# Optimization experiments

Hardware: AMD Instinct MI355X
Metric: run time of the kernel (lower is better)

The kernel has to match this reference:

```python
import jax, jax.numpy as jnp
import numpy as np

B, L, F, T = 512, 512, 128, 512

def setup_inputs() -> dict:
    key = jax.random.key(0)
    ks = jax.random.split(key, 8)
    s_ih = 1.0 / np.sqrt(L)
    return {
        "h0": jax.random.normal(ks[0], (1, B, L), jnp.float32),
        "c0": jax.random.normal(ks[1], (1, B, L), jnp.float32),
        "W_ih": jax.random.normal(ks[2], (4 * L, F), jnp.float32) * s_ih,
        "W_hh": jax.random.normal(ks[3], (4 * L, L), jnp.float32) * s_ih,
        "b_ih": jax.random.normal(ks[4], (4 * L,), jnp.float32) * s_ih,
        "b_hh": jax.random.normal(ks[5], (4 * L,), jnp.float32) * s_ih,
        "W_dense": jax.random.normal(ks[6], (F, L), jnp.float32) * s_ih,
        "b_dense": jax.random.normal(ks[7], (F,), jnp.float32) * s_ih,
        "seq_len": T,
    }

def reference(h0, c0, W_ih, W_hh, b_ih, b_hh, W_dense, b_dense, seq_len):
    h = h0[0]  # [B, L] (squeeze num_layers dim)
    c = c0[0]
    x = h @ W_dense.T + b_dense  # initial x_i = dense(h)

    def step(carry, _):
        x, h, c = carry
        gates = x @ W_ih.T + b_ih + h @ W_hh.T + b_hh  # [B, 4L]
        i, f, g, o = jnp.split(gates, 4, axis=-1)
        c2 = jax.nn.sigmoid(f) * c + jax.nn.sigmoid(i) * jnp.tanh(g)
        h2 = jax.nn.sigmoid(o) * jnp.tanh(c2)
        x2 = h2 @ W_dense.T + b_dense  # [B, F]
        return (x2, h2, c2), x2

    _, xs = jax.lax.scan(step, (x, h, c), None, length=seq_len)  # xs: [T, B, F]
    # torch code cats along axis=1 then views (-1, seq_len, n_features) -> [B, T, F]
    return jnp.transpose(xs, (1, 0, 2))
```

## Files before the change

kernel.cpp:

```cpp
#include <hip/hip_runtime.h>
#include <hip/hip_fp16.h>

#define T_STEPS 512
#define BDIM 512
#define LDIM 512
#define FDIM 128

typedef _Float16 half8 __attribute__((ext_vector_type(8)));
typedef float f4_t __attribute__((ext_vector_type(4)));

#define OFF_WPERM   0u
#define OFF_WDH     2097152u
#define OFF_BCOMB   2228224u
#define OFF_HBUF0   2236416u
#define OFF_HBUF1   2760704u
#define OFF_FLAGS   3284992u

__device__ __forceinline__ float sigmoidf_(float x) { return 1.f / (1.f + __expf(-x)); }
__device__ __forceinline__ float tanhf_(float x) { return 1.f - 2.f / (__expf(2.f * x) + 1.f); }

__device__ __forceinline__ void gload_lds16(const void* g, void* l) {
    __builtin_amdgcn_global_load_lds(
        (const __attribute__((address_space(1))) void*)g,
        (__attribute__((address_space(3))) void*)l, 16, 0, 0);
}

__device__ __forceinline__ unsigned long long aload64(const void* p) {
    return __hip_atomic_load((unsigned long long*)p, __ATOMIC_RELAXED, __HIP_MEMORY_SCOPE_AGENT);
}
__device__ __forceinline__ unsigned aload32(const void* p) {
    return __hip_atomic_load((unsigned*)p, __ATOMIC_RELAXED, __HIP_MEMORY_SCOPE_AGENT);
}
__device__ __forceinline__ void astore32(void* p, unsigned v) {
    __hip_atomic_store((unsigned*)p, v, __ATOMIC_RELAXED, __HIP_MEMORY_SCOPE_AGENT);
}

__global__ __launch_bounds__(256) void k_prep_w(
    const float* __restrict__ W_ih, const float* __restrict__ W_hh,
    const float* __restrict__ b_ih, const float* __restrict__ b_hh,
    const float* __restrict__ W_dense, const float* __restrict__ b_dense,
    _Float16* __restrict__ Wperm, float* __restrict__ bcomb)
{
    __shared__ float ih[FDIM];
    const int pr = blockIdx.x;
    const int gate = pr & 3, sg = pr >> 2;
    const int j = gate * 512 + sg;
    const int tid = threadIdx.x;
    if (tid < FDIM) ih[tid] = W_ih[j * FDIM + tid];
    __syncthreads();
    const int k0 = tid * 2;
    float a0 = W_hh[(size_t)j * LDIM + k0];
    float a1 = W_hh[(size_t)j * LDIM + k0 + 1];
    for (int f = 0; f < FDIM; ++f) {
        const float w = ih[f];
        a0 += w * W_dense[f * LDIM + k0];
        a1 += w * W_dense[f * LDIM + k0 + 1];
    }
    const int s = (pr & 7) << 6;
    Wperm[(size_t)pr * LDIM + (k0 ^ s)] = (_Float16)a0;
    Wperm[(size_t)pr * LDIM + (k0 ^ s) + 1] = (_Float16)a1;
    if (tid == 0) {
        float acc = b_ih[j] + b_hh[j];
        for (int f = 0; f < FDIM; ++f) acc += ih[f] * b_dense[f];
        bcomb[j] = acc;
    }
}

__global__ __launch_bounds__(256) void k_prep_misc(
    const float* __restrict__ W_dense, const float* __restrict__ h0,
    _Float16* __restrict__ Wdh, _Float16* __restrict__ hbuf0)
{
    const int bid = blockIdx.x, tid = threadIdx.x;
    const int k0 = tid * 2;
    if (bid < FDIM) {
        const int f = bid; const int s = (f & 7) << 6;
        Wdh[f * LDIM + (k0 ^ s)] = (_Float16)W_dense[f * LDIM + k0];
        Wdh[f * LDIM + (k0 ^ s) + 1] = (_Float16)W_dense[f * LDIM + k0 + 1];
    } else {
        const int r = bid - FDIM; const int s = (r & 7) << 6;
        hbuf0[r * LDIM + (k0 ^ s)] = (_Float16)h0[r * LDIM + k0];
        hbuf0[r * LDIM + (k0 ^ s) + 1] = (_Float16)h0[r * LDIM + k0 + 1];
    }
}

#define LDS_W   0
#define LDS_WD  65536
#define LDS_H   69632
#define LDS_TOT 135168

__device__ __forceinline__ void stage_h(char* smem, const char* gh, int tid) {
    #pragma unroll
    for (int ch = 0; ch < 4; ++ch) {
        unsigned long long tmp[8];
        #pragma unroll
        for (int r = 0; r < 8; ++r) tmp[r] = aload64(gh + ((ch * 8 + r) * 256 + tid) * 8);
        #pragma unroll
        for (int r = 0; r < 8; ++r)
            *(unsigned long long*)(smem + LDS_H + ((ch * 8 + r) * 256 + tid) * 8) = tmp[r];
    }
}

__global__ __launch_bounds__(256, 1) void k_persist(
    const _Float16* __restrict__ Wperm, const _Float16* __restrict__ Wdh,
    const float* __restrict__ bcomb, const float* __restrict__ bdense,
    const float* __restrict__ c0,
    _Float16* __restrict__ hb0, _Float16* __restrict__ hb1,
    float* __restrict__ out, unsigned* __restrict__ flags)
{
    __shared__ __align__(16) char smem[LDS_TOT];
    const int cb = blockIdx.x;
    const int g = blockIdx.y;
    const int tid = threadIdx.x;
    const int w = tid >> 6, lane = tid & 63;
    const int wm = w >> 1, wn = w & 1;
    const int lr = lane & 15, lh = lane >> 4;

    {
        const char* gw = (const char*)Wperm + (size_t)cb * 65536;
        #pragma unroll
        for (int i = 0; i < 16; ++i)
            gload_lds16(gw + (i * 256 + tid) * 16, smem + LDS_W + (i * 256 + tid) * 16);
        const char* gd = (const char*)Wdh + (size_t)cb * 4096;
        gload_lds16(gd + tid * 16, smem + LDS_WD + tid * 16);
    }

    float bi[2], bf[2], bg[2], bo[2];
    float creg[2][2];
    #pragma unroll
    for (int mt2 = 0; mt2 < 2; ++mt2) {
        const int sg = cb * 16 + 8 * wm + 4 * mt2 + lh;
        bi[mt2] = bcomb[0 * 512 + sg];
        bf[mt2] = bcomb[1 * 512 + sg];
        bg[mt2] = bcomb[2 * 512 + sg];
        bo[mt2] = bcomb[3 * 512 + sg];
        #pragma unroll
        for (int nt2 = 0; nt2 < 2; ++nt2) {
            const int row = g * 64 + (2 * wn + nt2) * 16 + lr;
            creg[mt2][nt2] = c0[(size_t)row * LDIM + sg];
        }
    }
    float bd[4];
    #pragma unroll
    for (int j = 0; j < 4; ++j) bd[j] = bdense[cb * 4 + j];

    const int ntx = 2 * wn + wm;
    const int swz = (lr & 7) << 7;
    const int swD = ((cb * 4 + lr) & 7) << 7;
    const char* pA0 = smem + LDS_W + ((2 * wm + 0) * 16 + lr) * 1024;
    const char* pA1 = smem + LDS_W + ((2 * wm + 1) * 16 + lr) * 1024;
    const char* pB0 = smem + LDS_H + ((2 * wn + 0) * 16 + lr) * 1024;
    const char* pB1 = smem + LDS_H + ((2 * wn + 1) * 16 + lr) * 1024;
    const char* pBx = smem + LDS_H + (ntx * 16 + lr) * 1024;
    const char* pD  = smem + LDS_WD + lr * 1024;

    unsigned* myflags = flags + g * 32;

    stage_h(smem, (const char*)hb0 + (size_t)g * 65536, tid);
    __syncthreads();

    half8 aA0[16], aA1[16], aD[16];
    #pragma unroll
    for (int kt = 0; kt < 16; ++kt) {
        const int kb = kt * 64 + lh * 16;
        aA0[kt] = *(const half8*)(pA0 + (kb ^ swz));
        aA1[kt] = *(const half8*)(pA1 + (kb ^ swz));
        aD[kt]  = *(const half8*)(pD  + (kb ^ swD));
    }

    for (int t = 1; t <= T_STEPS; ++t) {
        char* hout = (char*)((t & 1) ? hb1 : hb0);

        f4_t acc[2][2] = {};
        f4_t accx = {};
        #pragma unroll
        for (int kt = 0; kt < 16; ++kt) {
            const int kb = kt * 64 + lh * 16;
            const half8 b0 = *(const half8*)(pB0 + (kb ^ swz));
            const half8 b1 = *(const half8*)(pB1 + (kb ^ swz));
            acc[0][0] = __builtin_amdgcn_mfma_f32_16x16x32_f16(aA0[kt], b0, acc[0][0], 0, 0, 0);
            acc[0][1] = __builtin_amdgcn_mfma_f32_16x16x32_f16(aA0[kt], b1, acc[0][1], 0, 0, 0);
            acc[1][0] = __builtin_amdgcn_mfma_f32_16x16x32_f16(aA1[kt], b0, acc[1][0], 0, 0, 0);
            acc[1][1] = __builtin_amdgcn_mfma_f32_16x16x32_f16(aA1[kt], b1, acc[1][1], 0, 0, 0);
            accx = __builtin_amdgcn_mfma_f32_16x16x32_f16(aD[kt], wm ? b1 : b0, accx, 0, 0, 0);
        }

        #pragma unroll
        for (int mt2 = 0; mt2 < 2; ++mt2) {
            const int sg = cb * 16 + 8 * wm + 4 * mt2 + lh;
            #pragma unroll
            for (int nt2 = 0; nt2 < 2; ++nt2) {
                const int row = g * 64 + (2 * wn + nt2) * 16 + lr;
                const float iv = sigmoidf_(acc[mt2][nt2][0] + bi[mt2]);
                const float fv = sigmoidf_(acc[mt2][nt2][1] + bf[mt2]);
                const float gv = tanhf_(acc[mt2][nt2][2] + bg[mt2]);
                const float ov = sigmoidf_(acc[mt2][nt2][3] + bo[mt2]);
                const float cnew = fv * creg[mt2][nt2] + iv * gv;
                const float hnew = ov * tanhf_(cnew);
                creg[mt2][nt2] = cnew;
                const unsigned u = (unsigned)__builtin_bit_cast(unsigned short, (_Float16)hnew);
                const unsigned up = (unsigned)__shfl_xor((int)u, 16);
                if ((lh & 1) == 0) {
                    const unsigned word = u | (up << 16);
                    astore32(hout + row * 1024 + ((sg * 2) ^ ((row & 7) << 7)), word);
                }
            }
        }

        __syncthreads();
        if (tid == 0) astore32(myflags + cb, (unsigned)t);

        if (t >= 2 && lh == 0) {
            const int row = g * 64 + ntx * 16 + lr;
            float* o = &out[((size_t)row * T_STEPS + (t - 2)) * FDIM + cb * 4];
            o[0] = accx[0] + bd[0];
            o[1] = accx[1] + bd[1];
            o[2] = accx[2] + bd[2];
            o[3] = accx[3] + bd[3];
        }

        if (w == 0) {
            for (;;) {
                const unsigned v = (lane < 32) ? aload32(myflags + lane) : 0xffffffffu;
                if (__all(v >= (unsigned)t)) break;
                __builtin_amdgcn_s_sleep(1);
            }
        }
        __syncthreads();

        stage_h(smem, (const char*)((t & 1) ? hb1 : hb0) + (size_t)g * 65536, tid);
        __syncthreads();
    }

    {
        f4_t accx = {};
        #pragma unroll
        for (int kt = 0; kt < 16; ++kt) {
            const int kb = kt * 64 + lh * 16;
            const half8 b = *(const half8*)(pBx + (kb ^ swz));
            accx = __builtin_amdgcn_mfma_f32_16x16x32_f16(aD[kt], b, accx, 0, 0, 0);
        }
        if (lh == 0) {
            const int row = g * 64 + ntx * 16 + lr;
            float* o = &out[((size_t)row * T_STEPS + (T_STEPS - 1)) * FDIM + cb * 4];
            o[0] = accx[0] + bd[0];
            o[1] = accx[1] + bd[1];
            o[2] = accx[2] + bd[2];
            o[3] = accx[3] + bd[3];
        }
    }
}

extern "C" void kernel_launch(void* const* d_in, const int* in_sizes, int n_in,
                              void* d_out, int out_size, void* d_ws, size_t ws_size,
                              hipStream_t stream)
{
    const float* h0      = (const float*)d_in[0];
    const float* c0      = (const float*)d_in[1];
    const float* W_ih    = (const float*)d_in[2];
    const float* W_hh    = (const float*)d_in[3];
    const float* b_ih    = (const float*)d_in[4];
    const float* b_hh    = (const float*)d_in[5];
    const float* W_dense = (const float*)d_in[6];
    const float* b_dense = (const float*)d_in[7];
    float* out = (float*)d_out;
    char* ws = (char*)d_ws;

    _Float16* Wperm = (_Float16*)(ws + OFF_WPERM);
    _Float16* Wdh   = (_Float16*)(ws + OFF_WDH);
    float*    bcomb = (float*)(ws + OFF_BCOMB);
    _Float16* hb0   = (_Float16*)(ws + OFF_HBUF0);
    _Float16* hb1   = (_Float16*)(ws + OFF_HBUF1);
    unsigned* flags = (unsigned*)(ws + OFF_FLAGS);

    hipMemsetAsync(flags, 0, 1024, stream);
    k_prep_w<<<2048, 256, 0, stream>>>(W_ih, W_hh, b_ih, b_hh, W_dense, b_dense, Wperm, bcomb);
    k_prep_misc<<<FDIM + BDIM, 256, 0, stream>>>(W_dense, h0, Wdh, hb0);
    k_persist<<<dim3(32, 8), 256, 0, stream>>>(Wperm, Wdh, bcomb, b_dense, c0, hb0, hb1, out, flags);
}
```

Before: 2.838 ms.

## Replace block-wide barrier sync with per-wave flags and direct register h loads

Drops LDS staging of the hidden state and the two block-wide barriers per step. Each wave now owns 16 batch rows across all 64 gate columns and keeps the weights in registers. It waits on per-wave flags published by the 32 column blocks, then loads its h row directly from global memory in four chunks, pipelining the flag check and load of the next chunk behind the MFMAs on the current one. Chunk order is staggered by block to spread contention. The aim is finer-grained sync and less LDS traffic, at the cost of more register pressure and more global polling traffic.

After: 4.982 ms. +75.5%, slower.

```diff
diff --git a/kernel.cpp b/kernel.cpp
--- a/kernel.cpp
+++ b/kernel.cpp
@@ -8,6 +8,7 @@
 
 typedef _Float16 half8 __attribute__((ext_vector_type(8)));
 typedef float f4_t __attribute__((ext_vector_type(4)));
+typedef unsigned long long ull2 __attribute__((ext_vector_type(2)));
 
 #define OFF_WPERM   0u
 #define OFF_WDH     2097152u
@@ -19,17 +20,8 @@
 __device__ __forceinline__ float sigmoidf_(float x) { return 1.f / (1.f + __expf(-x)); }
 __device__ __forceinline__ float tanhf_(float x) { return 1.f - 2.f / (__expf(2.f * x) + 1.f); }
 
-__device__ __forceinline__ void gload_lds16(const void* g, void* l) {
-    __builtin_amdgcn_global_load_lds(
-        (const __attribute__((address_space(1))) void*)g,
-        (__attribute__((address_space(3))) void*)l, 16, 0, 0);
-}
-
 __device__ __forceinline__ unsigned long long aload64(const void* p) {
-    return __hip_atomic_load((unsigned long long*)p, __ATOMIC_RELAXED, __HIP_MEMORY_SCOPE_AGENT);
-}
-__device__ __forceinline__ unsigned aload32(const void* p) {
-    return __hip_atomic_load((unsigned*)p, __ATOMIC_RELAXED, __HIP_MEMORY_SCOPE_AGENT);
+    return __hip_atomic_load((const unsigned long long*)p, __ATOMIC_RELAXED, __HIP_MEMORY_SCOPE_AGENT);
 }
 __device__ __forceinline__ void astore32(void* p, unsigned v) {
     __hip_atomic_store((unsigned*)p, v, __ATOMIC_RELAXED, __HIP_MEMORY_SCOPE_AGENT);
@@ -83,23 +75,6 @@
     }
 }
 
-#define LDS_W   0
-#define LDS_WD  65536
-#define LDS_H   69632
-#define LDS_TOT 135168
-
-__device__ __forceinline__ void stage_h(char* smem, const char* gh, int tid) {
-    #pragma unroll
-    for (int ch = 0; ch < 4; ++ch) {
-        unsigned long long tmp[8];
-        #pragma unroll
-        for (int r = 0; r < 8; ++r) tmp[r] = aload64(gh + ((ch * 8 + r) * 256 + tid) * 8);
-        #pragma unroll
-        for (int r = 0; r < 8; ++r)
-            *(unsigned long long*)(smem + LDS_H + ((ch * 8 + r) * 256 + tid) * 8) = tmp[r];
-    }
-}
-
 __global__ __launch_bounds__(256, 1) void k_persist(
     const _Float16* __restrict__ Wperm, const _Float16* __restrict__ Wdh,
     const float* __restrict__ bcomb, const float* __restrict__ bdense,
@@ -107,140 +82,158 @@
     _Float16* __restrict__ hb0, _Float16* __restrict__ hb1,
     float* __restrict__ out, unsigned* __restrict__ flags)
 {
-    __shared__ __align__(16) char smem[LDS_TOT];
     const int cb = blockIdx.x;
     const int g = blockIdx.y;
     const int tid = threadIdx.x;
-    const int w = tid >> 6, lane = tid & 63;
-    const int wm = w >> 1, wn = w & 1;
+    const int wv = tid >> 6, lane = tid & 63;
     const int lr = lane & 15, lh = lane >> 4;
-
+    const int row = g * 64 + wv * 16 + lr;
+    const int swz = (lr & 7) << 7;
+    const int qs = cb >> 3;
+
+    half8 aA[4][16];
+    half8 aD[16];
     {
-        const char* gw = (const char*)Wperm + (size_t)cb * 65536;
-        #pragma unroll
-        for (int i = 0; i < 16; ++i)
-            gload_lds16(gw + (i * 256 + tid) * 16, smem + LDS_W + (i * 256 + tid) * 16);
-        const char* gd = (const char*)Wdh + (size_t)cb * 4096;
-        gload_lds16(gd + tid * 16, smem + LDS_WD + tid * 16);
-    }
-
-    float bi[2], bf[2], bg[2], bo[2];
-    float creg[2][2];
+        const char* wbase = (const char*)Wperm + (size_t)cb * 65536;
+        const int fd = cb * 4 + (lr & 3);
+        const char* dbase = (const char*)Wdh + (size_t)fd * 1024;
+        const int swD = (fd & 7) << 7;
+        #pragma unroll
+        for (int j = 0; j < 4; ++j) {
+            #pragma unroll
+            for (int cc = 0; cc < 4; ++cc) {
+                const int kt = ((qs + j) & 3) * 4 + cc;
+                const int kb = kt * 64 + lh * 16;
+                const int i = j * 4 + cc;
+                #pragma unroll
+                for (int m = 0; m < 4; ++m)
+                    aA[m][i] = *(const half8*)(wbase + (m * 16 + lr) * 1024 + (kb ^ swz));
+                aD[i] = *(const half8*)(dbase + (kb ^ swD));
+            }
+        }
+    }
+
+    float bi[4], bf[4], bg[4], bo[4], creg[4];
     #pragma unroll
-    for (int mt2 = 0; mt2 < 2; ++mt2) {
-        const int sg = cb * 16 + 8 * wm + 4 * mt2 + lh;
-        bi[mt2] = bcomb[0 * 512 + sg];
-        bf[mt2] = bcomb[1 * 512 + sg];
-        bg[mt2] = bcomb[2 * 512 + sg];
-        bo[mt2] = bcomb[3 * 512 + sg];
-        #pragma unroll
-        for (int nt2 = 0; nt2 < 2; ++nt2) {
-            const int row = g * 64 + (2 * wn + nt2) * 16 + lr;
-            creg[mt2][nt2] = c0[(size_t)row * LDIM + sg];
-        }
+    for (int m = 0; m < 4; ++m) {
+        const int sg = cb * 16 + m * 4 + lh;
+        bi[m] = bcomb[0 * 512 + sg];
+        bf[m] = bcomb[1 * 512 + sg];
+        bg[m] = bcomb[2 * 512 + sg];
+        bo[m] = bcomb[3 * 512 + sg];
+        creg[m] = c0[(size_t)row * LDIM + sg];
     }
     float bd[4];
     #pragma unroll
     for (int j = 0; j < 4; ++j) bd[j] = bdense[cb * 4 + j];
 
-    const int ntx = 2 * wn + wm;
-    const int swz = (lr & 7) << 7;
-    const int swD = ((cb * 4 + lr) & 7) << 7;
-    const char* pA0 = smem + LDS_W + ((2 * wm + 0) * 16 + lr) * 1024;
-    const char* pA1 = smem + LDS_W + ((2 * wm + 1) * 16 + lr) * 1024;
-    const char* pB0 = smem + LDS_H + ((2 * wn + 0) * 16 + lr) * 1024;
-    const char* pB1 = smem + LDS_H + ((2 * wn + 1) * 16 + lr) * 1024;
-    const char* pBx = smem + LDS_H + (ntx * 16 + lr) * 1024;
-    const char* pD  = smem + LDS_WD + lr * 1024;
-
-    unsigned* myflags = flags + g * 32;
-
-    stage_h(smem, (const char*)hb0 + (size_t)g * 65536, tid);
-    __syncthreads();
-
-    half8 aA0[16], aA1[16], aD[16];
-    #pragma unroll
-    for (int kt = 0; kt < 16; ++kt) {
-        const int kb = kt * 64 + lh * 16;
-        aA0[kt] = *(const half8*)(pA0 + (kb ^ swz));
-        aA1[kt] = *(const half8*)(pA1 + (kb ^ swz));
-        aD[kt]  = *(const half8*)(pD  + (kb ^ swD));
-    }
+    unsigned* fbase = flags + (g * 4 + wv) * 32;
+    const size_t rowoff = (size_t)row * 1024;
+
+    unsigned long long pf0, pf1, pf2, pf3;
+    ull2 bq[4], bn[4];
+
+#define FISSUE(q) do { const int qq_ = (q) & 3;                      \
+        pf0 = aload64(fbase + qq_ * 8 + 0);                          \
+        pf1 = aload64(fbase + qq_ * 8 + 2);                          \
+        pf2 = aload64(fbase + qq_ * 8 + 4);                          \
+        pf3 = aload64(fbase + qq_ * 8 + 6); } while (0)
+
+#define FCHECK(q, tw_) do { const int qq_ = (q) & 3;                 \
+        for (;;) {                                                   \
+            if ((unsigned)pf0 >= (tw_) && (unsigned)(pf0 >> 32) >= (tw_) && \
+                (unsigned)pf1 >= (tw_) && (unsigned)(pf1 >> 32) >= (tw_) && \
+                (unsigned)pf2 >= (tw_) && (unsigned)(pf2 >> 32) >= (tw_) && \
+                (unsigned)pf3 >= (tw_) && (unsigned)(pf3 >> 32) >= (tw_)) break; \
+            __builtin_amdgcn_s_sleep(1);                             \
+            pf0 = aload64(fbase + qq_ * 8 + 0);                      \
+            pf1 = aload64(fbase + qq_ * 8 + 2);                      \
+            pf2 = aload64(fbase + qq_ * 8 + 4);                      \
+            pf3 = aload64(fbase + qq_ * 8 + 6);                      \
+        } } while (0)
+
+#define BISSUE(q, dst) do { const int qq_ = (q) & 3;                 \
+        const unsigned dep_ = (unsigned)(((pf0 | pf1 | pf2 | pf3) >> 63) & 1ull); \
+        _Pragma("unroll")                                            \
+        for (int cc_ = 0; cc_ < 4; ++cc_) {                          \
+            const char* hp_ = hbase + rowoff + ((((qq_ * 4 + cc_) * 64 + lh * 16) ^ swz) + dep_); \
+            dst[cc_].x = aload64(hp_);                               \
+            dst[cc_].y = aload64(hp_ + 8); } } while (0)
 
     for (int t = 1; t <= T_STEPS; ++t) {
+        const char* hbase = (const char*)(((t - 1) & 1) ? hb1 : hb0);
         char* hout = (char*)((t & 1) ? hb1 : hb0);
-
-        f4_t acc[2][2] = {};
+        const unsigned tw = (unsigned)(t - 1);
+
+        f4_t acc[4] = {};
         f4_t accx = {};
-        #pragma unroll
-        for (int kt = 0; kt < 16; ++kt) {
-            const int kb = kt * 64 + lh * 16;
-            const half8 b0 = *(const half8*)(pB0 + (kb ^ swz));
-            const half8 b1 = *(const half8*)(pB1 + (kb ^ swz));
-            acc[0][0] = __builtin_amdgcn_mfma_f32_16x16x32_f16(aA0[kt], b0, acc[0][0], 0, 0, 0);
-            acc[0][1] = __builtin_amdgcn_mfma_f32_16x16x32_f16(aA0[kt], b1, acc[0][1], 0, 0, 0);
-            acc[1][0] = __builtin_amdgcn_mfma_f32_16x16x32_f16(aA1[kt], b0, acc[1][0], 0, 0, 0);
-            acc[1][1] = __builtin_amdgcn_mfma_f32_16x16x32_f16(aA1[kt], b1, acc[1][1], 0, 0, 0);
-            accx = __builtin_amdgcn_mfma_f32_16x16x32_f16(aD[kt], wm ? b1 : b0, accx, 0, 0, 0);
-        }
-
-        #pragma unroll
-        for (int mt2 = 0; mt2 < 2; ++mt2) {
-            const int sg = cb * 16 + 8 * wm + 4 * mt2 + lh;
+
+        FISSUE(qs); FCHECK(qs, tw); BISSUE(qs, bq);
+        FISSUE(qs + 1);
+
+        #pragma unroll
+        for (int j = 0; j < 4; ++j) {
+            if (j < 3) {
+                FCHECK(qs + j + 1, tw);
+                BISSUE(qs + j + 1, bn);
+                if (j < 2) FISSUE(qs + j + 2);
+            }
             #pragma unroll
-            for (int nt2 = 0; nt2 < 2; ++nt2) {
-                const int row = g * 64 + (2 * wn + nt2) * 16 + lr;
-                const float iv = sigmoidf_(acc[mt2][nt2][0] + bi[mt2]);
-                const float fv = sigmoidf_(acc[mt2][nt2][1] + bf[mt2]);
-                const float gv = tanhf_(acc[mt2][nt2][2] + bg[mt2]);
-                const float ov = sigmoidf_(acc[mt2][nt2][3] + bo[mt2]);
-                const float cnew = fv * creg[mt2][nt2] + iv * gv;
-                const float hnew = ov * tanhf_(cnew);
-                creg[mt2][nt2] = cnew;
-                const unsigned u = (unsigned)__builtin_bit_cast(unsigned short, (_Float16)hnew);
-                const unsigned up = (unsigned)__shfl_xor((int)u, 16);
-                if ((lh & 1) == 0) {
-                    const unsigned word = u | (up << 16);
-                    astore32(hout + row * 1024 + ((sg * 2) ^ ((row & 7) << 7)), word);
-                }
-            }
-        }
-
-        __syncthreads();
-        if (tid == 0) astore32(myflags + cb, (unsigned)t);
+            for (int cc = 0; cc < 4; ++cc) {
+                const half8 b = __builtin_bit_cast(half8, bq[cc]);
+                const int i = j * 4 + cc;
+                acc[0] = __builtin_amdgcn_mfma_f32_16x16x32_f16(aA[0][i], b, acc[0], 0, 0, 0);
+                acc[1] = __builtin_amdgcn_mfma_f32_16x16x32_f16(aA[1][i], b, acc[1], 0, 0, 0);
+                acc[2] = __builtin_amdgcn_mfma_f32_16x16x32_f16(aA[2][i], b, acc[2], 0, 0, 0);
+                acc[3] = __builtin_amdgcn_mfma_f32_16x16x32_f16(aA[3][i], b, acc[3], 0, 0, 0);
+                accx   = __builtin_amdgcn_mfma_f32_16x16x32_f16(aD[i],    b, accx,   0, 0, 0);
+            }
+            if (j < 3) { bq[0] = bn[0]; bq[1] = bn[1]; bq[2] = bn[2]; bq[3] = bn[3]; }
+        }
+
+        #pragma unroll
+        for (int m = 0; m < 4; ++m) {
+            const int sg = cb * 16 + m * 4 + lh;
+            const float iv = sigmoidf_(acc[m][0] + bi[m]);
+            const float fv = sigmoidf_(acc[m][1] + bf[m]);
+            const float gv = tanhf_(acc[m][2] + bg[m]);
+            const float ov = sigmoidf_(acc[m][3] + bo[m]);
+            const float cnew = fv * creg[m] + iv * gv;
+            const float hnew = ov * tanhf_(cnew);
+            creg[m] = cnew;
+            const unsigned u = (unsigned)__builtin_bit_cast(unsigned short, (_Float16)hnew);
+            const unsigned up = (unsigned)__shfl_xor((int)u, 16);
+            if ((lh & 1) == 0) {
+                astore32(hout + rowoff + ((sg * 2) ^ ((row & 7) << 7)), u | (up << 16));
+            }
+        }
+
+        asm volatile("s_waitcnt vmcnt(0)" ::: "memory");
+        if (lane == 0) astore32(fbase + cb, (unsigned)t);
 
         if (t >= 2 && lh == 0) {
-            const int row = g * 64 + ntx * 16 + lr;
             float* o = &out[((size_t)row * T_STEPS + (t - 2)) * FDIM + cb * 4];
             o[0] = accx[0] + bd[0];
             o[1] = accx[1] + bd[1];
             o[2] = accx[2] + bd[2];
             o[3] = accx[3] + bd[3];
         }
-
-        if (w == 0) {
-            for (;;) {
-                const unsigned v = (lane < 32) ? aload32(myflags + lane) : 0xffffffffu;
-                if (__all(v >= (unsigned)t)) break;
-                __builtin_amdgcn_s_sleep(1);
-            }
-        }
-        __syncthreads();
-
-        stage_h(smem, (const char*)((t & 1) ? hb1 : hb0) + (size_t)g * 65536, tid);
-        __syncthreads();
     }
 
     {
+        const unsigned tw = (unsigned)T_STEPS;
+        const char* hbase = (const char*)hb0;
         f4_t accx = {};
         #pragma unroll
-        for (int kt = 0; kt < 16; ++kt) {
-            const int kb = kt * 64 + lh * 16;
-            const half8 b = *(const half8*)(pBx + (kb ^ swz));
-            accx = __builtin_amdgcn_mfma_f32_16x16x32_f16(aD[kt], b, accx, 0, 0, 0);
+        for (int j = 0; j < 4; ++j) {
+            FISSUE(qs + j); FCHECK(qs + j, tw); BISSUE(qs + j, bq);
+            #pragma unroll
+            for (int cc = 0; cc < 4; ++cc) {
+                const half8 b = __builtin_bit_cast(half8, bq[cc]);
+                accx = __builtin_amdgcn_mfma_f32_16x16x32_f16(aD[j * 4 + cc], b, accx, 0, 0, 0);
+            }
         }
         if (lh == 0) {
-            const int row = g * 64 + ntx * 16 + lr;
             float* o = &out[((size_t)row * T_STEPS + (T_STEPS - 1)) * FDIM + cb * 4];
             o[0] = accx[0] + bd[0];
             o[1] = accx[1] + bd[1];
@@ -248,6 +241,9 @@
             o[3] = accx[3] + bd[3];
         }
     }
+#undef FISSUE
+#undef FCHECK
+#undef BISSUE
 }
 
 extern "C" void kernel_launch(void* const* d_in, const int* in_sizes, int n_in,
@@ -272,7 +268,7 @@
     _Float16* hb1   = (_Float16*)(ws + OFF_HBUF1);
     unsigned* flags = (unsigned*)(ws + OFF_FLAGS);
 
-    hipMemsetAsync(flags, 0, 1024, stream);
+    hipMemsetAsync(flags, 0, 4096, stream);
     k_prep_w<<<2048, 256, 0, stream>>>(W_ih, W_hh, b_ih, b_hh, W_dense, b_dense, Wperm, bcomb);
     k_prep_misc<<<FDIM + BDIM, 256, 0, stream>>>(W_dense, h0, Wdh, hb0);
     k_persist<<<dim3(32, 8), 256, 0, stream>>>(Wperm, Wdh, bcomb, b_dense, c0, hb0, hb1, out, flags);
```
